# Performance work log

Hardware: AMD Instinct MI355X
Metric: run time of the kernel (lower is better)

Reference implementation:

```python
import jax, jax.numpy as jnp
import numpy as np

INF = jnp.float32(jnp.inf)
# 8 grid directions (the torch module always uses all 8; self.diagonal is never read)
DIRS = jnp.array([[-1, 0], [1, 0], [0, -1], [0, 1],
                  [-1, -1], [-1, 1], [1, -1], [1, 1]], dtype=jnp.int32)


def setup_inputs() -> dict:
    key = jax.random.key(0)
    b, n = 128, 32
    weights = jax.random.uniform(key, (b, n, n), dtype=jnp.float32)
    return {"weights": weights}


def _dijkstra_path(weights):
    b, n, _ = weights.shape
    ar = jnp.arange(b)

    dist = jnp.full((b, n, n), INF, dtype=weights.dtype).at[:, 0, 0].set(0.0)
    vis = jnp.zeros((b, n, n), dtype=bool)
    pred = jnp.zeros((b, n, n, 2), dtype=jnp.int32)

    def relax_step(_, state):
        dist, vis, pred = state
        # pick unvisited node with minimum distance, per batch element
        unvis = jnp.where(vis, INF, dist)                       # (b, n, n)
        idx = jnp.argmin(unvis.reshape(b, -1), axis=1)          # (b,)
        cy, cx = idx // n, idx % n
        vis = vis.at[ar, cy, cx].set(True)
        cur = dist[ar, cy, cx]                                   # (b,)

        # 8 neighbors, vectorized over the direction axis
        ny = cy[:, None] + DIRS[None, :, 0]                      # (b, 8)
        nx = cx[:, None] + DIRS[None, :, 1]
        valid = (ny >= 0) & (ny < n) & (nx >= 0) & (nx < n)
        nyc = jnp.clip(ny, 0, n - 1)
        nxc = jnp.clip(nx, 0, n - 1)
        bb = jnp.broadcast_to(ar[:, None], (b, 8))

        old = dist[bb, nyc, nxc]
        nvis = vis[bb, nyc, nxc]
        new = cur[:, None] + weights[bb, nyc, nxc]
        upd = valid & ~nvis & (new < old)

        # duplicate-safe relaxation: scatter-min with inf where no update
        dist = dist.at[bb, nyc, nxc].min(jnp.where(upd, new, INF))
        # cells updated this step all get predecessor (cy, cx)
        umask = jnp.zeros((b, n, n), dtype=bool).at[bb, nyc, nxc].max(upd)
        cur_yx = jnp.stack([cy, cx], axis=-1)[:, None, None, :]  # (b,1,1,2)
        pred = jnp.where(umask[..., None], cur_yx.astype(pred.dtype), pred)
        return dist, vis, pred

    # Running the full n*n relaxations is equivalent to the torch early-break:
    # by Dijkstra's invariant, the target's distance/predecessor are final once
    # it would be popped, and later pops never alter the target path.
    dist, vis, pred = jax.lax.fori_loop(0, n * n, relax_step, (dist, vis, pred))

    # backtrack from (n-1, n-1) to (0, 0); pred[0,0] == (0,0) so it is a fixed point
    path = jnp.zeros((b, n, n), dtype=jnp.float32).at[:, n - 1, n - 1].set(1.0)

    def back_step(_, state):
        path, cy, cx = state
        py = pred[ar, cy, cx, 0]
        px = pred[ar, cy, cx, 1]
        path = path.at[ar, py, px].set(1.0)
        return path, py, px

    start = jnp.full((b,), n - 1, dtype=jnp.int32)
    path, _, _ = jax.lax.fori_loop(0, n * n, back_step, (path, start, start))
    return path


def reference(weights) -> jnp.ndarray:
    return _dijkstra_path(weights)
```

## Files before the change

kernel.cpp:

```cpp
#include <hip/hip_runtime.h>

#define N   32
#define NN  1024

__global__ __launch_bounds__(64, 1) void dijkstra_path_kernel(
    const float* __restrict__ weights, float* __restrict__ out)
{
    const int b    = blockIdx.x;
    const int lane = threadIdx.x & 63;
    const int ty   = lane >> 3;
    const int tx   = lane & 7;
    const int y0   = ty << 2;
    const int x0   = tx << 2;

    __shared__ int   pred[NN];
    __shared__ float pathf[NN];

    const float INF = __builtin_huge_valf();

    #pragma unroll
    for (int k = 0; k < 16; ++k) pathf[lane + k * 64] = 0.0f;

    float w[4][4];
    const float* wb = weights + b * NN;
    #pragma unroll
    for (int i = 0; i < 4; ++i) {
        const float4 v = *(const float4*)(wb + (y0 + i) * N + x0);
        w[i][0] = v.x; w[i][1] = v.y; w[i][2] = v.z; w[i][3] = v.w;
    }

    float g[6][6];
    #pragma unroll
    for (int i = 0; i < 6; ++i)
        #pragma unroll
        for (int j = 0; j < 6; ++j) g[i][j] = INF;
    if (lane == 0) g[1][1] = 0.0f;

    const bool hT = (ty > 0), hB = (ty < 7), hL = (tx > 0), hR = (tx < 7);

#define EXCHANGE()                                                            \
    {                                                                         \
        float tT[4], tB[4], tL[4], tR[4];                                     \
        _Pragma("unroll")                                                     \
        for (int j = 0; j < 4; ++j) tT[j] = __shfl(g[4][1 + j], lane - 8);    \
        _Pragma("unroll")                                                     \
        for (int j = 0; j < 4; ++j) tB[j] = __shfl(g[1][1 + j], lane + 8);    \
        _Pragma("unroll")                                                     \
        for (int i = 0; i < 4; ++i) tL[i] = __shfl(g[1 + i][4], lane - 1);    \
        _Pragma("unroll")                                                     \
        for (int i = 0; i < 4; ++i) tR[i] = __shfl(g[1 + i][1], lane + 1);    \
        const float cTL = __shfl(g[4][4], lane - 9);                          \
        const float cTR = __shfl(g[4][1], lane - 7);                          \
        const float cBL = __shfl(g[1][4], lane + 7);                          \
        const float cBR = __shfl(g[1][1], lane + 9);                          \
        _Pragma("unroll")                                                     \
        for (int j = 0; j < 4; ++j) {                                         \
            g[0][1 + j] = hT ? tT[j] : INF;                                   \
            g[5][1 + j] = hB ? tB[j] : INF;                                   \
        }                                                                     \
        _Pragma("unroll")                                                     \
        for (int i = 0; i < 4; ++i) {                                         \
            g[1 + i][0] = hL ? tL[i] : INF;                                   \
            g[1 + i][5] = hR ? tR[i] : INF;                                   \
        }                                                                     \
        g[0][0] = (hT && hL) ? cTL : INF;                                     \
        g[0][5] = (hT && hR) ? cTR : INF;                                     \
        g[5][0] = (hB && hL) ? cBL : INF;                                     \
        g[5][5] = (hB && hR) ? cBR : INF;                                     \
    }

#define RELAX(i, j)                                                           \
    {                                                                         \
        const float old = g[(i)][(j)];                                        \
        const float a = fminf(fminf(g[(i)-1][(j)-1], g[(i)-1][(j)]),          \
                              g[(i)-1][(j)+1]);                               \
        const float c = fminf(fminf(g[(i)][(j)-1], g[(i)][(j)+1]),            \
                              g[(i)+1][(j)-1]);                               \
        const float e = fminf(g[(i)+1][(j)], g[(i)+1][(j)+1]);                \
        const float m = fminf(fminf(a, c), e);                                \
        const float nv = m + w[(i)-1][(j)-1];                                 \
        changed |= (nv < old);                                                \
        g[(i)][(j)] = fminf(old, nv);                                         \
    }

    for (int it = 0; it < 384; ++it) {
        bool changed = false;
        EXCHANGE()
        #pragma unroll
        for (int i = 1; i <= 4; ++i)
            #pragma unroll
            for (int j = 1; j <= 4; ++j) RELAX(i, j)
        changed = false;
        EXCHANGE()
        #pragma unroll
        for (int i = 4; i >= 1; --i)
            #pragma unroll
            for (int j = 4; j >= 1; --j) RELAX(i, j)
        if (!__any((int)changed)) break;
    }
#undef RELAX
#undef EXCHANGE

    const int dy[8] = {-1, 1, 0, 0, -1, -1, 1, 1};
    const int dx[8] = { 0, 0,-1, 1, -1,  1,-1, 1};
    #pragma unroll
    for (int i = 0; i < 4; ++i)
        #pragma unroll
        for (int j = 0; j < 4; ++j) {
            const int yy = y0 + i, xx = x0 + j;
            const int t  = yy * N + xx;
            int p = 0;
            if (t != 0) {
                float best = INF;
                #pragma unroll
                for (int k = 0; k < 8; ++k) {
                    const float u = g[1 + i + dy[k]][1 + j + dx[k]];
                    const float c = u + w[i][j];
                    if (c < best) { best = c; p = (yy + dy[k]) * N + (xx + dx[k]); }
                }
            }
            pred[t] = p;
        }
    __threadfence_block();

    if (lane == 0) {
        int cur = NN - 1;
        pathf[cur] = 1.0f;
        for (int s = 0; s < NN && cur != 0; ++s) {
            cur = pred[cur];
            pathf[cur] = 1.0f;
        }
    }
    __threadfence_block();

    float* ob = out + b * NN;
    #pragma unroll
    for (int i = 0; i < 4; ++i) {
        const int t = (y0 + i) * N + x0;
        const float4 v = *(const float4*)&pathf[t];
        *(float4*)(ob + t) = v;
    }
}

extern "C" void kernel_launch(void* const* d_in, const int* in_sizes, int n_in,
                              void* d_out, int out_size, void* d_ws, size_t ws_size,
                              hipStream_t stream) {
    const float* w = (const float*)d_in[0];
    float* out = (float*)d_out;
    const int b = in_sizes[0] / NN;
    dijkstra_path_kernel<<<dim3(b), dim3(64), 0, stream>>>(w, out);
}
```

Measured before the change: 71.73 us.

## Use four diagonal sweep directions with per-sweep convergence checks in relaxation

```diff
diff --git a/kernel.cpp b/kernel.cpp
--- a/kernel.cpp
+++ b/kernel.cpp
@@ -69,58 +69,82 @@
         g[5][5] = (hB && hR) ? cBR : INF;                                     \
     }
 
-#define RELAX(i, j)                                                           \
+#define RELAXD(i, j, FI, FJ)                                                  \
     {                                                                         \
         const float old = g[(i)][(j)];                                        \
-        const float a = fminf(fminf(g[(i)-1][(j)-1], g[(i)-1][(j)]),          \
-                              g[(i)-1][(j)+1]);                               \
-        const float c = fminf(fminf(g[(i)][(j)-1], g[(i)][(j)+1]),            \
-                              g[(i)+1][(j)-1]);                               \
-        const float e = fminf(g[(i)+1][(j)], g[(i)+1][(j)+1]);                \
-        const float m = fminf(fminf(a, c), e);                                \
-        const float nv = m + w[(i)-1][(j)-1];                                 \
+        const float fr  = fminf(fminf(g[(i)+(FI)][(j)-1], g[(i)+(FI)][(j)]),  \
+                                g[(i)+(FI)][(j)+1]);                          \
+        const float st  = fminf(fminf(fminf(g[(i)-(FI)][(j)-1],               \
+                                            g[(i)-(FI)][(j)]),                \
+                                      g[(i)-(FI)][(j)+1]),                    \
+                                g[(i)][(j)-(FJ)]);                            \
+        const float nv  = fminf(fminf(st, fr), g[(i)][(j)+(FJ)])              \
+                          + w[(i)-1][(j)-1];                                  \
         changed |= (nv < old);                                                \
         g[(i)][(j)] = fminf(old, nv);                                         \
     }
 
-    for (int it = 0; it < 384; ++it) {
-        bool changed = false;
+    for (int it = 0; it < 192; ++it) {
+        bool changed;
+
         EXCHANGE()
+        changed = false;
         #pragma unroll
         for (int i = 1; i <= 4; ++i)
             #pragma unroll
-            for (int j = 1; j <= 4; ++j) RELAX(i, j)
+            for (int j = 1; j <= 4; ++j) RELAXD(i, j, -1, -1)
+        if (!__any((int)changed)) goto solved;
+
+        EXCHANGE()
         changed = false;
+        #pragma unroll
+        for (int i = 1; i <= 4; ++i)
+            #pragma unroll
+            for (int j = 4; j >= 1; --j) RELAXD(i, j, -1, +1)
+        if (!__any((int)changed)) goto solved;
+
         EXCHANGE()
+        changed = false;
         #pragma unroll
         for (int i = 4; i >= 1; --i)
             #pragma unroll
-            for (int j = 4; j >= 1; --j) RELAX(i, j)
-        if (!__any((int)changed)) break;
+            for (int j = 4; j >= 1; --j) RELAXD(i, j, +1, +1)
+        if (!__any((int)changed)) goto solved;
+
+        EXCHANGE()
+        changed = false;
+        #pragma unroll
+        for (int i = 4; i >= 1; --i)
+            #pragma unroll
+            for (int j = 1; j <= 4; ++j) RELAXD(i, j, +1, -1)
+        if (!__any((int)changed)) goto solved;
     }
-#undef RELAX
+solved:
+#undef RELAXD
 #undef EXCHANGE
 
-    const int dy[8] = {-1, 1, 0, 0, -1, -1, 1, 1};
-    const int dx[8] = { 0, 0,-1, 1, -1,  1,-1, 1};
-    #pragma unroll
-    for (int i = 0; i < 4; ++i)
+    {
+        const int dy[8] = {-1, 1, 0, 0, -1, -1, 1, 1};
+        const int dx[8] = { 0, 0,-1, 1, -1,  1,-1, 1};
         #pragma unroll
-        for (int j = 0; j < 4; ++j) {
-            const int yy = y0 + i, xx = x0 + j;
-            const int t  = yy * N + xx;
-            int p = 0;
-            if (t != 0) {
-                float best = INF;
-                #pragma unroll
-                for (int k = 0; k < 8; ++k) {
-                    const float u = g[1 + i + dy[k]][1 + j + dx[k]];
-                    const float c = u + w[i][j];
-                    if (c < best) { best = c; p = (yy + dy[k]) * N + (xx + dx[k]); }
+        for (int i = 0; i < 4; ++i)
+            #pragma unroll
+            for (int j = 0; j < 4; ++j) {
+                const int yy = y0 + i, xx = x0 + j;
+                const int t  = yy * N + xx;
+                int p = 0;
+                if (t != 0) {
+                    float best = INF;
+                    #pragma unroll
+                    for (int k = 0; k < 8; ++k) {
+                        const float u = g[1 + i + dy[k]][1 + j + dx[k]];
+                        const float c = u + w[i][j];
+                        if (c < best) { best = c; p = (yy + dy[k]) * N + (xx + dx[k]); }
+                    }
                 }
+                pred[t] = p;
             }
-            pred[t] = p;
-        }
+    }
     __threadfence_block();
 
     if (lane == 0) {
```

New measurement: 73.27 us. 2.1% more time.
